# Kernel optimization log

Measured on AMD Instinct MI355X. Metric: run time of the kernel, lower is better.

Reference implementation:

```python
import math
import jax, jax.numpy as jnp
import numpy as np

D_MODEL = 2048
HEAD = 128
DEPTH = 12
LAMBDA_INIT = 0.8 - 0.6 * math.exp(-0.3 * DEPTH)
RMS_EPS = float(np.finfo(np.float32).eps)  # torch RMSNorm default eps=None -> finfo.eps


def setup_inputs() -> dict:
    key = jax.random.key(0)
    ks = jax.random.split(key, 9)
    B, S = 2, 4096
    std_l = 0.1
    return {
        "x": jax.random.normal(ks[0], (B, S, D_MODEL), dtype=jnp.float32),
        "Wq": jax.random.normal(ks[1], (HEAD, D_MODEL), dtype=jnp.float32) / math.sqrt(D_MODEL),
        "Wk": jax.random.normal(ks[2], (HEAD, D_MODEL), dtype=jnp.float32) / math.sqrt(D_MODEL),
        "Wv": jax.random.normal(ks[3], (HEAD, D_MODEL), dtype=jnp.float32) / math.sqrt(D_MODEL),
        "lambda_q1": std_l * jax.random.normal(ks[4], (HEAD // 2,), dtype=jnp.float32),
        "lambda_q2": std_l * jax.random.normal(ks[5], (HEAD // 2,), dtype=jnp.float32),
        "lambda_k1": std_l * jax.random.normal(ks[6], (HEAD // 2,), dtype=jnp.float32),
        "lambda_k2": std_l * jax.random.normal(ks[7], (HEAD // 2,), dtype=jnp.float32),
        "rms_weight": jnp.ones((HEAD,), dtype=jnp.float32),
    }


def reference(x, Wq, Wk, Wv, lambda_q1, lambda_q2, lambda_k1, lambda_k2, rms_weight):
    # projections (torch Linear: x @ W.T)
    q = jnp.einsum("bsd,hd->bsh", x, Wq)
    k = jnp.einsum("bsd,hd->bsh", x, Wk)
    v = jnp.einsum("bsd,hd->bsh", x, Wv)
    h2 = HEAD // 2
    q1, q2 = q[..., :h2], q[..., h2:]
    k1, k2 = k[..., :h2], k[..., h2:]
    scale = 1.0 / math.sqrt(h2)
    attn1 = jax.nn.softmax(jnp.einsum("bqh,bkh->bqk", q1, k1) * scale, axis=-1)
    attn2 = jax.nn.softmax(jnp.einsum("bqh,bkh->bqk", q2, k2) * scale, axis=-1)
    lam = jnp.exp(jnp.dot(lambda_q1, lambda_k1)) - jnp.exp(jnp.dot(lambda_q2, lambda_k2)) + LAMBDA_INIT
    attn_out = jnp.einsum("bqk,bkh->bqh", attn1 - lam * attn2, v)
    # RMSNorm over last dim
    rms = jax.lax.rsqrt(jnp.mean(attn_out * attn_out, axis=-1, keepdims=True) + RMS_EPS)
    return (1.0 - LAMBDA_INIT) * (attn_out * rms * rms_weight)
```

## Files before the change

### kernel.cpp

```cpp
#include <hip/hip_runtime.h>
#include <hip/hip_bf16.h>
#include <math.h>

#define S_LEN 4096
#define DMODEL 2048
#define HEADD 128

typedef __attribute__((ext_vector_type(8))) short short8;
typedef __attribute__((ext_vector_type(4))) float floatx4;

__device__ __forceinline__ short f2bs(float f) {
  __hip_bfloat16 h = __float2bfloat16(f);
  short s; __builtin_memcpy(&s, &h, 2); return s;
}
__device__ __forceinline__ float bs2f(short s) {
  unsigned u = ((unsigned)(unsigned short)s) << 16;
  float f; __builtin_memcpy(&f, &u, 4); return f;
}
__device__ __forceinline__ int pkbf(float a, float b) {
  return (int)(((unsigned)(unsigned short)f2bs(b) << 16) |
               (unsigned)(unsigned short)f2bs(a));
}

__global__ __launch_bounds__(256) void convw_kernel(const float* __restrict__ wq,
                                                    const float* __restrict__ wk,
                                                    const float* __restrict__ wv,
                                                    short* __restrict__ wc) {
  const int per = 128 * 2048;
  int e = (blockIdx.x * blockDim.x + threadIdx.x) * 4;
  const float* src = (e < per) ? wq : (e < 2 * per) ? wk : wv;
  int off = e & (per - 1);
  float4 v = *(const float4*)(src + off);
  short4 r;
  r.x = f2bs(v.x); r.y = f2bs(v.y); r.z = f2bs(v.z); r.w = f2bs(v.w);
  *(short4*)(wc + e) = r;
}

__global__ __launch_bounds__(256, 3) void proj_kernel(const float* __restrict__ x,
                                                      const short* __restrict__ wc,
                                                      short* __restrict__ qm,
                                                      short* __restrict__ kb,
                                                      short* __restrict__ vstage) {
  const int tid = threadIdx.x;
  const int w = tid >> 6;
  const int lane = tid & 63;
  const int lo = lane & 15, g = lane >> 4;
  const int id = blockIdx.x;
  const int nq = id >> 7, mb = id & 127;
  const int m0 = mb * 64;
  const int n0 = nq * 96;

  __shared__ short xt[2][64 * 64];
  __shared__ short wt[2][96 * 64];

  const int r8 = tid >> 3, sc = tid & 7;
  const float* xs0 = x + (size_t)(m0 + r8) * DMODEL + sc * 8;
  const float* xs1 = x + (size_t)(m0 + 32 + r8) * DMODEL + sc * 8;
  const short* ws0 = wc + (size_t)(n0 + r8) * DMODEL + sc * 8;
  const short* ws1 = wc + (size_t)(n0 + 32 + r8) * DMODEL + sc * 8;
  const short* ws2 = wc + (size_t)(n0 + 64 + r8) * DMODEL + sc * 8;
  const int xl0 = r8 * 64 + ((sc ^ (r8 & 7)) * 8);
  const int xl1 = (32 + r8) * 64 + ((sc ^ (r8 & 7)) * 8);
  const int wlo0 = r8 * 64 + ((sc ^ (r8 & 7)) * 8);
  const int wlo1 = (32 + r8) * 64 + ((sc ^ (r8 & 7)) * 8);
  const int wlo2 = (64 + r8) * 64 + ((sc ^ (r8 & 7)) * 8);

  const int mrow = (w >> 1) * 32;
  const int ncol = (w & 1) * 48;
  int aoff[2][2], boff[3][2];
#pragma unroll
  for (int mi = 0; mi < 2; ++mi) {
    int r = mrow + mi * 16 + lo;
#pragma unroll
    for (int kc = 0; kc < 2; ++kc)
      aoff[mi][kc] = r * 64 + (((kc * 4 + g) ^ (r & 7)) * 8);
  }
#pragma unroll
  for (int t = 0; t < 3; ++t) {
    int r = ncol + t * 16 + lo;
#pragma unroll
    for (int kc = 0; kc < 2; ++kc)
      boff[t][kc] = r * 64 + (((kc * 4 + g) ^ (r & 7)) * 8);
  }

  floatx4 acc[2][3];
#pragma unroll
  for (int mi = 0; mi < 2; ++mi)
#pragma unroll
    for (int t = 0; t < 3; ++t) acc[mi][t] = floatx4{0.f, 0.f, 0.f, 0.f};

  {
    float4 a0 = *(const float4*)(xs0), a1 = *(const float4*)(xs0 + 4);
    float4 b0 = *(const float4*)(xs1), b1 = *(const float4*)(xs1 + 4);
    int4 w0 = *(const int4*)(ws0);
    int4 w1 = *(const int4*)(ws1);
    int4 w2 = *(const int4*)(ws2);
    short8 sA, sB;
    sA[0]=f2bs(a0.x); sA[1]=f2bs(a0.y); sA[2]=f2bs(a0.z); sA[3]=f2bs(a0.w);
    sA[4]=f2bs(a1.x); sA[5]=f2bs(a1.y); sA[6]=f2bs(a1.z); sA[7]=f2bs(a1.w);
    sB[0]=f2bs(b0.x); sB[1]=f2bs(b0.y); sB[2]=f2bs(b0.z); sB[3]=f2bs(b0.w);
    sB[4]=f2bs(b1.x); sB[5]=f2bs(b1.y); sB[6]=f2bs(b1.z); sB[7]=f2bs(b1.w);
    *(short8*)&xt[0][xl0] = sA;
    *(short8*)&xt[0][xl1] = sB;
    *(int4*)&wt[0][wlo0] = w0;
    *(int4*)&wt[0][wlo1] = w1;
    *(int4*)&wt[0][wlo2] = w2;
  }
  __syncthreads();

  int cur = 0;
#pragma unroll 1
  for (int it = 0; it < 32; ++it) {
    float4 a0, a1, b0, b1;
    int4 w0, w1, w2;
    if (it + 1 < 32) {
      const int k = (it + 1) * 64;
      a0 = *(const float4*)(xs0 + k); a1 = *(const float4*)(xs0 + k + 4);
      b0 = *(const float4*)(xs1 + k); b1 = *(const float4*)(xs1 + k + 4);
      w0 = *(const int4*)(ws0 + k);
      w1 = *(const int4*)(ws1 + k);
      w2 = *(const int4*)(ws2 + k);
    }

    {
      const short* xb = &xt[cur][0];
      const short* wb = &wt[cur][0];
      short8 af[2][2], bf[3][2];
#pragma unroll
      for (int mi = 0; mi < 2; ++mi)
#pragma unroll
        for (int kc = 0; kc < 2; ++kc) af[mi][kc] = *(const short8*)(xb + aoff[mi][kc]);
#pragma unroll
      for (int t = 0; t < 3; ++t)
#pragma unroll
        for (int kc = 0; kc < 2; ++kc) bf[t][kc] = *(const short8*)(wb + boff[t][kc]);
#pragma unroll
      for (int kc = 0; kc < 2; ++kc)
#pragma unroll
        for (int mi = 0; mi < 2; ++mi)
#pragma unroll
          for (int t = 0; t < 3; ++t)
            acc[mi][t] = __builtin_amdgcn_mfma_f32_16x16x32_bf16(af[mi][kc], bf[t][kc], acc[mi][t], 0, 0, 0);
    }

    if (it + 1 < 32) {
      short8 sA, sB;
      sA[0]=f2bs(a0.x); sA[1]=f2bs(a0.y); sA[2]=f2bs(a0.z); sA[3]=f2bs(a0.w);
      sA[4]=f2bs(a1.x); sA[5]=f2bs(a1.y); sA[6]=f2bs(a1.z); sA[7]=f2bs(a1.w);
      sB[0]=f2bs(b0.x); sB[1]=f2bs(b0.y); sB[2]=f2bs(b0.z); sB[3]=f2bs(b0.w);
      sB[4]=f2bs(b1.x); sB[5]=f2bs(b1.y); sB[6]=f2bs(b1.z); sB[7]=f2bs(b1.w);
      *(short8*)&xt[cur ^ 1][xl0] = sA;
      *(short8*)&xt[cur ^ 1][xl1] = sB;
      *(int4*)&wt[cur ^ 1][wlo0] = w0;
      *(int4*)&wt[cur ^ 1][wlo1] = w1;
      *(int4*)&wt[cur ^ 1][wlo2] = w2;
    }
    __syncthreads();
    cur ^= 1;
  }

#pragma unroll
  for (int t = 0; t < 3; ++t) {
    int n = n0 + ncol + t * 16 + lo;
#pragma unroll
    for (int mi = 0; mi < 2; ++mi)
#pragma unroll
      for (int j = 0; j < 4; ++j) {
        int m = m0 + mrow + mi * 16 + g * 4 + j;
        float v = acc[mi][t][j];
        if (n < HEADD) {
          qm[(size_t)m * HEADD + n] = f2bs(v * 0.125f);
        } else if (n < 2 * HEADD) {
          kb[(size_t)m * HEADD + (n - HEADD)] = f2bs(v);
        } else {
          vstage[(size_t)m * HEADD + (n - 2 * HEADD)] = f2bs(v);
        }
      }
  }
}

__global__ __launch_bounds__(256) void conv_v_kernel(const short* __restrict__ vstage,
                                                     short* __restrict__ vt) {
  const int tid = threadIdx.x;
  const int bb = blockIdx.x >> 6, st = blockIdx.x & 63;
  const int s0 = st * 64;

  __shared__ short ld[64][136];

  const int r = tid >> 2, c8 = (tid & 3) * 32;
#pragma unroll
  for (int q = 0; q < 4; ++q) {
    const size_t off = (size_t)(bb * 4096 + s0 + r) * 128 + c8 + q * 8;
    *(short8*)(&ld[r][c8 + q * 8]) = *(const short8*)(vstage + off);
  }
  __syncthreads();

  const int h = tid >> 1, sh = (tid & 1) * 32;
#pragma unroll
  for (int q = 0; q < 4; ++q) {
    short8 t;
#pragma unroll
    for (int i = 0; i < 8; ++i) t[i] = ld[sh + q * 8 + i][h];
    *(short8*)(vt + ((size_t)bb * 128 + h) * 4096 + s0 + sh + q * 8) = t;
  }
}

__global__ __launch_bounds__(256, 3) void attn_kernel(const short* __restrict__ qm,
                                                      const short* __restrict__ kb,
                                                      const short* __restrict__ vt,
                                                      short* __restrict__ po,
                                                      float* __restrict__ pls) {
  const int tid = threadIdx.x;
  const int w = tid >> 6;
  const int lane = tid & 63;
  const int lo = lane & 15, g = lane >> 4;
  const int qsp = w >> 1;
  const int s = w & 1;
  const int id = blockIdx.x;
  const int ksp = id & 7;
  const int qblk = id >> 3;
  const int b = qblk >> 6;
  const int kv_base = ksp * 512;

  __shared__ short kt[2][32 * 128];
  __shared__ short vl[2][128 * 32];

  const int kr0 = tid >> 4, kck = tid & 15;
  const int vr0 = tid >> 2, vck = tid & 3;
  const short* kS = kb + (size_t)b * S_LEN * HEADD;
  const short* vS = vt + (size_t)b * HEADD * S_LEN;
  const int kld0 = kr0 * 128 + ((kck ^ (kr0 & 7)) * 8);
  const int kld1 = (kr0 + 16) * 128 + ((kck ^ (kr0 & 7)) * 8);
  const int vld0 = vr0 * 32 + ((vck ^ (vr0 & 3)) * 8);
  const int vld1 = (vr0 + 64) * 32 + ((vck ^ (vr0 & 3)) * 8);

  const int rowqA = qblk * 64 + qsp * 32;
  const int rowqB = rowqA + 16;
  const short* qrowA = qm + (size_t)(rowqA + lo) * HEADD + s * 64;
  const short* qrowB = qm + (size_t)(rowqB + lo) * HEADD + s * 64;
  const short8 qA0 = *(const short8*)(qrowA + g * 8);
  const short8 qA1 = *(const short8*)(qrowA + 32 + g * 8);
  const short8 qB0 = *(const short8*)(qrowB + g * 8);
  const short8 qB1 = *(const short8*)(qrowB + 32 + g * 8);

  floatx4 accA[8], accB[8];
#pragma unroll
  for (int n = 0; n < 8; ++n) {
    accA[n] = floatx4{0.f, 0.f, 0.f, 0.f};
    accB[n] = floatx4{0.f, 0.f, 0.f, 0.f};
  }
  float lxA = 0.f, lxB = 0.f;

  const int kc0 = ((s * 8 + g) ^ (lo & 7)) * 8;
  const int kc1 = ((s * 8 + 4 + g) ^ (lo & 7)) * 8;
  const int kro0 = lo * 128, kro1 = (16 + lo) * 128;
  const int vco = (g ^ (lo & 3)) * 8;

  const int gA = (g & 1) * 2;
  const int idx0 = lo + 16 * gA, idx1 = idx0 + 16;
  const bool hi = (g >= 2);

  {
    int4 ka = *(const int4*)(kS + (size_t)(kv_base + kr0) * HEADD + kck * 8);
    int4 kbx = *(const int4*)(kS + (size_t)(kv_base + kr0 + 16) * HEADD + kck * 8);
    int4 va = *(const int4*)(vS + (size_t)vr0 * S_LEN + kv_base + vck * 8);
    int4 vb = *(const int4*)(vS + (size_t)(vr0 + 64) * S_LEN + kv_base + vck * 8);
    *(int4*)(&kt[0][kld0]) = ka;
    *(int4*)(&kt[0][kld1]) = kbx;
    *(int4*)(&vl[0][vld0]) = va;
    *(int4*)(&vl[0][vld1]) = vb;
  }
  __syncthreads();

  int cur = 0;
#pragma unroll 1
  for (int it = 0; it < 16; ++it) {
    int4 ka, kbx, va, vb;
    if (it + 1 < 16) {
      const int kvn = kv_base + (it + 1) * 32;
      ka  = *(const int4*)(kS + (size_t)(kvn + kr0) * HEADD + kck * 8);
      kbx = *(const int4*)(kS + (size_t)(kvn + kr0 + 16) * HEADD + kck * 8);
      va  = *(const int4*)(vS + (size_t)vr0 * S_LEN + kvn + vck * 8);
      vb  = *(const int4*)(vS + (size_t)(vr0 + 64) * S_LEN + kvn + vck * 8);
    }

    const short* kbase = &kt[cur][0];
    short8 a00 = *(const short8*)(kbase + kro0 + kc0);
    short8 a01 = *(const short8*)(kbase + kro0 + kc1);
    short8 a10 = *(const short8*)(kbase + kro1 + kc0);
    short8 a11 = *(const short8*)(kbase + kro1 + kc1);

    floatx4 z = floatx4{0.f, 0.f, 0.f, 0.f};
    floatx4 u;
    u = __builtin_amdgcn_mfma_f32_16x16x32_bf16(a00, qA0, z, 0, 0, 0);
    floatx4 T0A = __builtin_amdgcn_mfma_f32_16x16x32_bf16(a01, qA1, u, 0, 0, 0);
    u = __builtin_amdgcn_mfma_f32_16x16x32_bf16(a10, qA0, z, 0, 0, 0);
    floatx4 T1A = __builtin_amdgcn_mfma_f32_16x16x32_bf16(a11, qA1, u, 0, 0, 0);
    u = __builtin_amdgcn_mfma_f32_16x16x32_bf16(a00, qB0, z, 0, 0, 0);
    floatx4 T0B = __builtin_amdgcn_mfma_f32_16x16x32_bf16(a01, qB1, u, 0, 0, 0);
    u = __builtin_amdgcn_mfma_f32_16x16x32_bf16(a10, qB0, z, 0, 0, 0);
    floatx4 T1B = __builtin_amdgcn_mfma_f32_16x16x32_bf16(a11, qB1, u, 0, 0, 0);

    short8 paA, paB;
    {
      float p0 = __expf(T0A[0]), p1 = __expf(T0A[1]), p2 = __expf(T0A[2]), p3 = __expf(T0A[3]);
      float p4 = __expf(T1A[0]), p5 = __expf(T1A[1]), p6 = __expf(T1A[2]), p7 = __expf(T1A[3]);
      float lp = ((p0 + p1) + (p2 + p3)) + ((p4 + p5) + (p6 + p7));
      lp += __shfl_xor(lp, 16);
      lp += __shfl_xor(lp, 32);
      lxA += lp;
      int c00 = pkbf(p0, p1), c01 = pkbf(p2, p3);
      int c10 = pkbf(p4, p5), c11 = pkbf(p6, p7);
      int t0a = __shfl(c00, idx0), t0b = __shfl(c01, idx0);
      int t0c = __shfl(c00, idx1), t0d = __shfl(c01, idx1);
      int t1a = __shfl(c10, idx0), t1b = __shfl(c11, idx0);
      int t1c = __shfl(c10, idx1), t1d = __shfl(c11, idx1);
      int w0 = hi ? t1a : t0a, w1 = hi ? t1b : t0b;
      int w2 = hi ? t1c : t0c, w3 = hi ? t1d : t0d;
      int4 tmp = {w0, w1, w2, w3}; __builtin_memcpy(&paA, &tmp, 16);
    }
    {
      float p0 = __expf(T0B[0]), p1 = __expf(T0B[1]), p2 = __expf(T0B[2]), p3 = __expf(T0B[3]);
      float p4 = __expf(T1B[0]), p5 = __expf(T1B[1]), p6 = __expf(T1B[2]), p7 = __expf(T1B[3]);
      float lp = ((p0 + p1) + (p2 + p3)) + ((p4 + p5) + (p6 + p7));
      lp += __shfl_xor(lp, 16);
      lp += __shfl_xor(lp, 32);
      lxB += lp;
      int c00 = pkbf(p0, p1), c01 = pkbf(p2, p3);
      int c10 = pkbf(p4, p5), c11 = pkbf(p6, p7);
      int t0a = __shfl(c00, idx0), t0b = __shfl(c01, idx0);
      int t0c = __shfl(c00, idx1), t0d = __shfl(c01, idx1);
      int t1a = __shfl(c10, idx0), t1b = __shfl(c11, idx0);
      int t1c = __shfl(c10, idx1), t1d = __shfl(c11, idx1);
      int w0 = hi ? t1a : t0a, w1 = hi ? t1b : t0b;
      int w2 = hi ? t1c : t0c, w3 = hi ? t1d : t0d;
      int4 tmp = {w0, w1, w2, w3}; __builtin_memcpy(&paB, &tmp, 16);
    }

    const short* vbase = &vl[cur][0];
#pragma unroll
    for (int n = 0; n < 8; ++n) {
      short8 vf = *(const short8*)(vbase + (n * 16 + lo) * 32 + vco);
      accA[n] = __builtin_amdgcn_mfma_f32_16x16x32_bf16(paA, vf, accA[n], 0, 0, 0);
      accB[n] = __builtin_amdgcn_mfma_f32_16x16x32_bf16(paB, vf, accB[n], 0, 0, 0);
    }

    if (it + 1 < 16) {
      *(int4*)(&kt[cur ^ 1][kld0]) = ka;
      *(int4*)(&kt[cur ^ 1][kld1]) = kbx;
      *(int4*)(&vl[cur ^ 1][vld0]) = va;
      *(int4*)(&vl[cur ^ 1][vld1]) = vb;
    }
    __syncthreads();
    cur ^= 1;
  }

  short* pw = po + ((size_t)(ksp * 2 + s) * 8192) * 128;
#pragma unroll
  for (int j = 0; j < 4; ++j) {
    short8 pk;
#pragma unroll
    for (int n = 0; n < 8; ++n) pk[n] = f2bs(accA[n][j]);
    *(short8*)(pw + (size_t)(rowqA + g * 4 + j) * 128 + lo * 8) = pk;
#pragma unroll
    for (int n = 0; n < 8; ++n) pk[n] = f2bs(accB[n][j]);
    *(short8*)(pw + (size_t)(rowqB + g * 4 + j) * 128 + lo * 8) = pk;
  }
  if (g == 0) {
    pls[(size_t)(ksp * 2 + s) * 8192 + rowqA + lo] = lxA;
    pls[(size_t)(ksp * 2 + s) * 8192 + rowqB + lo] = lxB;
  }
}

__global__ __launch_bounds__(256) void merge_kernel(const short* __restrict__ po,
                                                    const float* __restrict__ pls,
                                                    const float* __restrict__ lq1,
                                                    const float* __restrict__ lq2,
                                                    const float* __restrict__ lk1,
                                                    const float* __restrict__ lk2,
                                                    const float* __restrict__ rmsw,
                                                    float* __restrict__ out) {
  const int tid = threadIdx.x;
  const int row = blockIdx.x * 16 + (tid >> 4);
  const int lo = tid & 15;

  float a1s = 0.f, a2s = 0.f;
  for (int i = 0; i < 64; ++i) {
    a1s = fmaf(lq1[i], lk1[i], a1s);
    a2s = fmaf(lq2[i], lk2[i], a2s);
  }
  const float lam = __expf(a1s) - __expf(a2s) + 0.7836057665316245f;

  float o1[8], o2[8];
#pragma unroll
  for (int n = 0; n < 8; ++n) { o1[n] = 0.f; o2[n] = 0.f; }
  float l1 = 0.f, l2 = 0.f;
#pragma unroll
  for (int ksp = 0; ksp < 8; ++ksp) {
    short8 sa = *(const short8*)(po + ((size_t)(ksp * 2 + 0) * 8192 + row) * 128 + lo * 8);
    short8 sb = *(const short8*)(po + ((size_t)(ksp * 2 + 1) * 8192 + row) * 128 + lo * 8);
#pragma unroll
    for (int n = 0; n < 8; ++n) { o1[n] += bs2f(sa[n]); o2[n] += bs2f(sb[n]); }
    l1 += pls[(size_t)(ksp * 2 + 0) * 8192 + row];
    l2 += pls[(size_t)(ksp * 2 + 1) * 8192 + row];
  }
  const float iL1 = 1.f / l1, iL2 = 1.f / l2;

  float v[8];
  float ssq = 0.f;
#pragma unroll
  for (int n = 0; n < 8; ++n) {
    v[n] = o1[n] * iL1 - lam * (o2[n] * iL2);
    ssq += v[n] * v[n];
  }
  ssq += __shfl_xor(ssq, 1);
  ssq += __shfl_xor(ssq, 2);
  ssq += __shfl_xor(ssq, 4);
  ssq += __shfl_xor(ssq, 8);
  const float rr = rsqrtf(ssq * (1.f / 128.f) + 1.1920928955078125e-07f);

  float* ob = out + (size_t)row * 128;
#pragma unroll
  for (int n = 0; n < 8; ++n) {
    int c = n * 16 + lo;
    ob[c] = 0.21639423346837554f * v[n] * rr * rmsw[c];
  }
}

extern "C" void kernel_launch(void* const* d_in, const int* in_sizes, int n_in,
                              void* d_out, int out_size, void* d_ws, size_t ws_size,
                              hipStream_t stream) {
  const float* x   = (const float*)d_in[0];
  const float* wq  = (const float*)d_in[1];
  const float* wk  = (const float*)d_in[2];
  const float* wv  = (const float*)d_in[3];
  const float* lq1 = (const float*)d_in[4];
  const float* lq2 = (const float*)d_in[5];
  const float* lk1 = (const float*)d_in[6];
  const float* lk2 = (const float*)d_in[7];
  const float* rw  = (const float*)d_in[8];
  float* out = (float*)d_out;

  char* ws = (char*)d_ws;
  short* qm  = (short*)(ws);
  short* kb  = (short*)(ws + (2u << 20));
  short* vt  = (short*)(ws + (4u << 20));
  short* wc  = (short*)(ws + (6u << 20));
  short* vstage = (short*)(ws + (6u << 20) + 1572864u);
  short* po  = (short*)(ws + (8u << 20));
  float* pls = (float*)(ws + (40u << 20));

  convw_kernel<<<768, 256, 0, stream>>>(wq, wk, wv, wc);
  proj_kernel<<<512, 256, 0, stream>>>(x, wc, qm, kb, vstage);
  conv_v_kernel<<<128, 256, 0, stream>>>(vstage, vt);
  attn_kernel<<<1024, 256, 0, stream>>>(qm, kb, vt, po, pls);
  merge_kernel<<<512, 256, 0, stream>>>(po, pls, lq1, lq2, lk1, lk2, rw, out);
}
```

Before: 97.16 us.

## Double attention block to 512 threads covering 128 query rows per K/V tile

The attention kernel now launches 512-thread blocks, each handling 128 query rows instead of 64, so every shared-memory K/V tile is reused by eight waves rather than four. Each thread now loads half as many K/V vectors per stage, which halves global K/V traffic per query row. In exchange the grid drops from 1024 to 512 blocks and occupancy per CU is capped at two larger blocks, so barrier stalls involve more waves and there may be fewer blocks available to balance across CUs.

```diff
diff --git a/kernel.cpp b/kernel.cpp
--- a/kernel.cpp
+++ b/kernel.cpp
@@ -205,7 +205,7 @@
   }
 }
 
-__global__ __launch_bounds__(256, 3) void attn_kernel(const short* __restrict__ qm,
+__global__ __launch_bounds__(512, 2) void attn_kernel(const short* __restrict__ qm,
                                                       const short* __restrict__ kb,
                                                       const short* __restrict__ vt,
                                                       short* __restrict__ po,
@@ -219,22 +219,20 @@
   const int id = blockIdx.x;
   const int ksp = id & 7;
   const int qblk = id >> 3;
-  const int b = qblk >> 6;
+  const int b = qblk >> 5;
   const int kv_base = ksp * 512;
 
   __shared__ short kt[2][32 * 128];
   __shared__ short vl[2][128 * 32];
 
-  const int kr0 = tid >> 4, kck = tid & 15;
-  const int vr0 = tid >> 2, vck = tid & 3;
+  const int kr = tid >> 4, kck = tid & 15;
+  const int vr = tid >> 2, vck = tid & 3;
   const short* kS = kb + (size_t)b * S_LEN * HEADD;
   const short* vS = vt + (size_t)b * HEADD * S_LEN;
-  const int kld0 = kr0 * 128 + ((kck ^ (kr0 & 7)) * 8);
-  const int kld1 = (kr0 + 16) * 128 + ((kck ^ (kr0 & 7)) * 8);
-  const int vld0 = vr0 * 32 + ((vck ^ (vr0 & 3)) * 8);
-  const int vld1 = (vr0 + 64) * 32 + ((vck ^ (vr0 & 3)) * 8);
-
-  const int rowqA = qblk * 64 + qsp * 32;
+  const int kld = kr * 128 + ((kck ^ (kr & 7)) * 8);
+  const int vld = vr * 32 + ((vck ^ (vr & 3)) * 8);
+
+  const int rowqA = qblk * 128 + qsp * 32;
   const int rowqB = rowqA + 16;
   const short* qrowA = qm + (size_t)(rowqA + lo) * HEADD + s * 64;
   const short* qrowB = qm + (size_t)(rowqB + lo) * HEADD + s * 64;
@@ -261,27 +259,21 @@
   const bool hi = (g >= 2);
 
   {
-    int4 ka = *(const int4*)(kS + (size_t)(kv_base + kr0) * HEADD + kck * 8);
-    int4 kbx = *(const int4*)(kS + (size_t)(kv_base + kr0 + 16) * HEADD + kck * 8);
-    int4 va = *(const int4*)(vS + (size_t)vr0 * S_LEN + kv_base + vck * 8);
-    int4 vb = *(const int4*)(vS + (size_t)(vr0 + 64) * S_LEN + kv_base + vck * 8);
-    *(int4*)(&kt[0][kld0]) = ka;
-    *(int4*)(&kt[0][kld1]) = kbx;
-    *(int4*)(&vl[0][vld0]) = va;
-    *(int4*)(&vl[0][vld1]) = vb;
+    int4 ka = *(const int4*)(kS + (size_t)(kv_base + kr) * HEADD + kck * 8);
+    int4 va = *(const int4*)(vS + (size_t)vr * S_LEN + kv_base + vck * 8);
+    *(int4*)(&kt[0][kld]) = ka;
+    *(int4*)(&vl[0][vld]) = va;
   }
   __syncthreads();
 
   int cur = 0;
 #pragma unroll 1
   for (int it = 0; it < 16; ++it) {
-    int4 ka, kbx, va, vb;
+    int4 ka, va;
     if (it + 1 < 16) {
       const int kvn = kv_base + (it + 1) * 32;
-      ka  = *(const int4*)(kS + (size_t)(kvn + kr0) * HEADD + kck * 8);
-      kbx = *(const int4*)(kS + (size_t)(kvn + kr0 + 16) * HEADD + kck * 8);
-      va  = *(const int4*)(vS + (size_t)vr0 * S_LEN + kvn + vck * 8);
-      vb  = *(const int4*)(vS + (size_t)(vr0 + 64) * S_LEN + kvn + vck * 8);
+      ka = *(const int4*)(kS + (size_t)(kvn + kr) * HEADD + kck * 8);
+      va = *(const int4*)(vS + (size_t)vr * S_LEN + kvn + vck * 8);
     }
 
     const short* kbase = &kt[cur][0];
@@ -346,10 +338,8 @@
     }
 
     if (it + 1 < 16) {
-      *(int4*)(&kt[cur ^ 1][kld0]) = ka;
-      *(int4*)(&kt[cur ^ 1][kld1]) = kbx;
-      *(int4*)(&vl[cur ^ 1][vld0]) = va;
-      *(int4*)(&vl[cur ^ 1][vld1]) = vb;
+      *(int4*)(&kt[cur ^ 1][kld]) = ka;
+      *(int4*)(&vl[cur ^ 1][vld]) = va;
     }
     __syncthreads();
     cur ^= 1;
@@ -453,6 +443,6 @@
   convw_kernel<<<768, 256, 0, stream>>>(wq, wk, wv, wc);
   proj_kernel<<<512, 256, 0, stream>>>(x, wc, qm, kb, vstage);
   conv_v_kernel<<<128, 256, 0, stream>>>(vstage, vt);
-  attn_kernel<<<1024, 256, 0, stream>>>(qm, kb, vt, po, pls);
+  attn_kernel<<<512, 512, 0, stream>>>(qm, kb, vt, po, pls);
   merge_kernel<<<512, 256, 0, stream>>>(po, pls, lq1, lq2, lk1, lk2, rw, out);
 }
```

Result: slower. 104.0 us (+7.0%).
